# Optimization experiments

Hardware: AMD Instinct MI355X
Metric: run time of the kernel (lower is better)

Reference implementation:

```python
import jax, jax.numpy as jnp
import numpy as np

HIDDEN = 1024
HEADS = 16
HEAD_DIM = HIDDEN // HEADS
B, S = 2, 2048


def setup_inputs() -> dict:
    key = jax.random.key(0)
    k1, k2, k3 = jax.random.split(key, 3)
    scale_in = 1.0 / np.sqrt(HIDDEN)
    x = jax.random.normal(k1, (B, S, HIDDEN), dtype=jnp.float32)
    wqkv_w = jax.random.normal(k2, (3 * HIDDEN, HIDDEN), dtype=jnp.float32) * scale_in
    wo_w = jax.random.normal(k3, (HIDDEN, HIDDEN), dtype=jnp.float32) * scale_in
    wo_b = jnp.zeros((HIDDEN,), dtype=jnp.float32)
    return {"x": x, "wqkv_w": wqkv_w, "wo_w": wo_w, "wo_b": wo_b}


def reference(x, wqkv_w, wo_w, wo_b):
    b, s, d = x.shape
    h, hd = HEADS, HEAD_DIM
    sm_scale = hd ** (-0.5)
    # QKV projection (torch Linear: x @ W^T), then chunk into q,k,v
    qkv = jnp.einsum('bsd,ed->bse', x, wqkv_w)  # [b, s, 3d]
    q, k, v = jnp.split(qkv, 3, axis=-1)
    # [b, h, s, hd]
    q = q.reshape(b, s, h, hd).transpose(0, 2, 1, 3)
    k = k.reshape(b, s, h, hd).transpose(0, 2, 1, 3)
    v = v.reshape(b, s, h, hd).transpose(0, 2, 1, 3)
    # raw scores, then causal mask (mask applied BEFORE scaling, as in source;
    # -inf * scale == -inf so math matches softmax(score*scale) with mask)
    scores = jnp.einsum('bhqe,bhke->bhqk', q, k)
    causal = jnp.tril(jnp.ones((s, s), dtype=bool))
    scores = jnp.where(causal[None, None, :, :], scores, -jnp.inf)
    weights = jax.nn.softmax(scores * sm_scale, axis=-1)
    # dropout p=0.0 (eval) -> identity
    out = jnp.einsum('bhqk,bhke->bhqe', weights, v)
    out = out.transpose(0, 2, 1, 3).reshape(b, s, h * hd)
    y = jnp.einsum('bsd,ed->bse', out, wo_w) + wo_b
    return (y, k, v)
```

## Files before the change

### kernel.cpp

```cpp
#include <hip/hip_runtime.h>
#include <cstdint>
#include <cstddef>


using bf16x8 = __attribute__((ext_vector_type(8))) __bf16;
using f32x4  = __attribute__((ext_vector_type(4))) float;
using u16    = unsigned short;

#define SOFT_SCALE 0.1803368801111244f

__device__ __forceinline__ u16 f2bf(float f) {
  union { float f; uint32_t u; } a; a.f = f;
  uint32_t r = a.u + 0x7fffu + ((a.u >> 16) & 1u);
  return (u16)(r >> 16);
}

__device__ __forceinline__ bf16x8 ldfrag(const u16* p) {
  return *reinterpret_cast<const bf16x8*>(p);
}

__device__ __forceinline__ void gload_lds16(const void* g, void* l) {
  __builtin_amdgcn_global_load_lds((const __attribute__((address_space(1))) void*)g,
                                   (__attribute__((address_space(3))) void*)l,
                                   16, 0, 0);
}

__device__ __forceinline__ uint32_t cvt_pk_bf16(float a, float b) {
  uint32_t r;
  asm("v_cvt_pk_bf16_f32 %0, %1, %2" : "=v"(r) : "v"(a), "v"(b));
  return r;
}

__global__ void cvt_all(const float* __restrict__ x, const float* __restrict__ wqkv,
                        const float* __restrict__ wo,
                        u16* __restrict__ xb, u16* __restrict__ wqkvb, u16* __restrict__ wob) {
  int i = blockIdx.x * blockDim.x + threadIdx.x;
  int stride = gridDim.x * blockDim.x;
  for (; i < 2097152; i += stride) {
    const float* src; u16* dst; int j;
    if (i < 1048576)      { src = x;    dst = xb;    j = i; }
    else if (i < 1835008) { src = wqkv; dst = wqkvb; j = i - 1048576; }
    else                  { src = wo;   dst = wob;   j = i - 1835008; }
    float4 v = reinterpret_cast<const float4*>(src)[j];
    ushort4 o;
    o.x = f2bf(v.x); o.y = f2bf(v.y); o.z = f2bf(v.z); o.w = f2bf(v.w);
    reinterpret_cast<ushort4*>(dst)[j] = o;
  }
}

__global__ __launch_bounds__(512, 2) void qkv_gemm_kernel(
    const u16* __restrict__ Xb, const u16* __restrict__ Wb,
    u16* __restrict__ Qws, u16* __restrict__ Kws, u16* __restrict__ Vtws,
    float* __restrict__ out) {
  extern __shared__ char smem[];

  const int tid = threadIdx.x, lane = tid & 63, wid = tid >> 6;
  const int wr = wid >> 2, wc = wid & 3;
  const int fq = lane >> 4, fr = lane & 15;

  const int wg = (blockIdx.x & 7) * 64 + (blockIdx.x >> 3);
  const int bm = wg >> 4, bn = wg & 15;
  const int m0 = bm * 128, n0 = bn * 192;

  const char* Ab = (const char*)Xb + (size_t)m0 * 2048;
  const char* Bb = (const char*)Wb + (size_t)n0 * 2048;

  f32x4 acc[4][3] = {};

  auto stage_A = [&](int t, int h) {
    char* dst = smem + (t & 1) * 16384 + h * 8192;
    int lin = tid * 16;
    int rl  = lin >> 7;
    int col = (lin & 127) ^ ((rl & 7) << 4);
    gload_lds16(Ab + (size_t)(h * 64 + rl) * 2048 + t * 128 + col, dst + lin);
  };
  auto stage_B = [&](int t) {
    char* dst = smem + 32768 + (t & 1) * 24576;
#pragma unroll
    for (int l = 0; l < 3; ++l) {
      int lin = (l * 512 + tid) * 16;
      int rl  = lin >> 7;
      int col = (lin & 127) ^ ((rl & 7) << 4);
      gload_lds16(Bb + (size_t)rl * 2048 + t * 128 + col, dst + lin);
    }
  };

  stage_A(0, 0); stage_A(0, 1);
  stage_B(0);
  stage_B(1);
  asm volatile("s_waitcnt vmcnt(3)" ::: "memory");
  __builtin_amdgcn_s_barrier();

  bf16x8 afr[2][2];
  bf16x8 bfr[3][2];

  for (int t = 0; t < 16; ++t) {
    const char* As = smem + (t & 1) * 16384;
    const char* Bs = smem + 32768 + (t & 1) * 24576;

#pragma unroll
    for (int m = 0; m < 2; ++m) {
      int row = wr * 64 + m * 16 + fr;
#pragma unroll
      for (int ks = 0; ks < 2; ++ks)
        afr[m][ks] = *(const bf16x8*)(As + row * 128 + ((ks * 64 + fq * 16) ^ ((row & 7) << 4)));
    }
#pragma unroll
    for (int n = 0; n < 3; ++n) {
      int row = wc * 48 + n * 16 + fr;
#pragma unroll
      for (int ks = 0; ks < 2; ++ks)
        bfr[n][ks] = *(const bf16x8*)(Bs + row * 128 + ((ks * 64 + fq * 16) ^ ((row & 7) << 4)));
    }
    if (t + 1 < 16) stage_A(t + 1, 0);
    __builtin_amdgcn_s_barrier();
    asm volatile("s_waitcnt lgkmcnt(0)" ::: "memory");
    __builtin_amdgcn_sched_barrier(0);
    __builtin_amdgcn_s_setprio(1);
#pragma unroll
    for (int m = 0; m < 2; ++m)
#pragma unroll
      for (int n = 0; n < 3; ++n)
#pragma unroll
        for (int ks = 0; ks < 2; ++ks)
          acc[m][n] = __builtin_amdgcn_mfma_f32_16x16x32_bf16(afr[m][ks], bfr[n][ks], acc[m][n], 0, 0, 0);
    __builtin_amdgcn_s_setprio(0);
    __builtin_amdgcn_s_barrier();

#pragma unroll
    for (int m = 0; m < 2; ++m) {
      int row = wr * 64 + (m + 2) * 16 + fr;
#pragma unroll
      for (int ks = 0; ks < 2; ++ks)
        afr[m][ks] = *(const bf16x8*)(As + row * 128 + ((ks * 64 + fq * 16) ^ ((row & 7) << 4)));
    }
    if (t + 1 < 16) stage_A(t + 1, 1);
    if (t + 2 < 16) stage_B(t + 2);
    __builtin_amdgcn_s_barrier();
    asm volatile("s_waitcnt lgkmcnt(0)" ::: "memory");
    __builtin_amdgcn_sched_barrier(0);
    __builtin_amdgcn_s_setprio(1);
#pragma unroll
    for (int m = 0; m < 2; ++m)
#pragma unroll
      for (int n = 0; n < 3; ++n)
#pragma unroll
        for (int ks = 0; ks < 2; ++ks)
          acc[m + 2][n] = __builtin_amdgcn_mfma_f32_16x16x32_bf16(afr[m][ks], bfr[n][ks], acc[m + 2][n], 0, 0, 0);
    __builtin_amdgcn_s_setprio(0);
    if (t < 14)       asm volatile("s_waitcnt vmcnt(3)" ::: "memory");
    else if (t == 14) asm volatile("s_waitcnt vmcnt(0)" ::: "memory");
    __builtin_amdgcn_s_barrier();
  }

  const int mbase = m0 + wr * 64;
#pragma unroll
  for (int m = 0; m < 4; ++m)
#pragma unroll
    for (int n = 0; n < 3; ++n) {
      int mB = mbase + m * 16 + fq * 4;
      int ncol = n0 + wc * 48 + n * 16 + fr;
      int sect = ncol >> 10;
      int nn = ncol & 1023;
      int b = mB >> 11, s0 = mB & 2047;
      int h = nn >> 6, hd = nn & 63;
      size_t base = (((size_t)b * 16 + h) * 2048 + s0) * 64 + hd;
      float v0 = acc[m][n][0], v1 = acc[m][n][1], v2 = acc[m][n][2], v3 = acc[m][n][3];
      if (sect == 0) {
        Qws[base]       = f2bf(v0 * SOFT_SCALE);
        Qws[base + 64]  = f2bf(v1 * SOFT_SCALE);
        Qws[base + 128] = f2bf(v2 * SOFT_SCALE);
        Qws[base + 192] = f2bf(v3 * SOFT_SCALE);
      } else if (sect == 1) {
        Kws[base] = f2bf(v0); Kws[base + 64] = f2bf(v1);
        Kws[base + 128] = f2bf(v2); Kws[base + 192] = f2bf(v3);
        out[4194304 + base] = v0; out[4194304 + base + 64] = v1;
        out[4194304 + base + 128] = v2; out[4194304 + base + 192] = v3;
      } else {
        out[8388608 + base] = v0; out[8388608 + base + 64] = v1;
        out[8388608 + base + 128] = v2; out[8388608 + base + 192] = v3;
        size_t tt = ((size_t)(b * 16 + h) * 64 + hd) * 2048 + s0;
        ushort4 pk; pk.x = f2bf(v0); pk.y = f2bf(v1); pk.z = f2bf(v2); pk.w = f2bf(v3);
        *reinterpret_cast<ushort4*>(Vtws + tt) = pk;
      }
    }
}

__device__ __forceinline__ void gemm128_core(const u16* __restrict__ A,
                                             const u16* __restrict__ B,
                                             int m0, int n0, int K,
                                             u16* As, u16* Bs, f32x4 acc[4][4]) {
  const int tid  = threadIdx.x;
  const int lane = tid & 63;
  const int wid  = tid >> 6;
  const int wr = wid >> 1, wc = wid & 1;
  const int fq = lane >> 4, fr = lane & 15;

  for (int kb = 0; kb < K; kb += 32) {
#pragma unroll
    for (int j = 0; j < 2; ++j) {
      int lin = (j * 256 + tid) * 16;
      int row = lin >> 6;
      int rb  = lin & 63;
      gload_lds16((const char*)(A + (size_t)(m0 + row) * K + kb) + rb, (char*)As + lin);
      gload_lds16((const char*)(B + (size_t)(n0 + row) * K + kb) + rb, (char*)Bs + lin);
    }
    __syncthreads();

    bf16x8 av[4], bv[4];
#pragma unroll
    for (int i = 0; i < 4; ++i) av[i] = ldfrag(As + (wr * 64 + i * 16 + fr) * 32 + fq * 8);
#pragma unroll
    for (int j = 0; j < 4; ++j) bv[j] = ldfrag(Bs + (wc * 64 + j * 16 + fr) * 32 + fq * 8);
    __builtin_amdgcn_s_setprio(1);
#pragma unroll
    for (int i = 0; i < 4; ++i)
#pragma unroll
      for (int j = 0; j < 4; ++j)
        acc[i][j] = __builtin_amdgcn_mfma_f32_16x16x32_bf16(av[i], bv[j], acc[i][j], 0, 0, 0);
    __builtin_amdgcn_s_setprio(0);
    __syncthreads();
  }
}

__global__ __launch_bounds__(256, 4) void attn_kernel(
    const u16* __restrict__ Qw, const u16* __restrict__ Kw,
    const u16* __restrict__ Vtw, u16* __restrict__ Ow) {
  __shared__ u16 Ks[2][64 * 64];
  __shared__ u16 Vs[2][64 * 64];

  const int tid = threadIdx.x, lane = tid & 63, wid = tid >> 6;
  const int wk = wid >> 1, wh = wid & 1;
  const int fq = lane >> 4, fr = lane & 15;
  const int bh = blockIdx.x & 31;
  const int qb = 31 - (blockIdx.x >> 5);
  const int b = bh >> 4, h = bh & 15;
  const int q0 = qb * 64;

  const u16* Qbase  = Qw  + (size_t)bh * 2048 * 64;
  const u16* Kbase  = Kw  + (size_t)bh * 2048 * 64;
  const char* VtBase = (const char*)(Vtw + (size_t)bh * 64 * 2048);

#pragma unroll
  for (int f = 0; f < 2; ++f) {
    int lin = (f * 256 + tid) * 16;
    int row = lin >> 7;
    int logical = lin ^ ((row & 7) << 4);
    gload_lds16((const char*)Kbase + logical, (char*)Ks[0] + lin);
    gload_lds16(VtBase + (size_t)row * 4096 + (logical & 127), (char*)Vs[0] + lin);
  }

  bf16x8 qa[2][2];
#pragma unroll
  for (int qt = 0; qt < 2; ++qt)
#pragma unroll
    for (int kh = 0; kh < 2; ++kh)
      qa[qt][kh] = ldfrag(Qbase + (size_t)(q0 + wh * 32 + qt * 16 + fr) * 64 + kh * 32 + fq * 8);

  float ssum[2] = {0.f, 0.f};
  f32x4 accO[2][4] = {};

  int cur = 0;
  for (int kb = 0; kb <= qb; ++kb) {
    __syncthreads();

    if (kb < qb) {
      const char* kg = (const char*)(Kbase + (size_t)(kb + 1) * 64 * 64);
#pragma unroll
      for (int f = 0; f < 2; ++f) {
        int lin = (f * 256 + tid) * 16;
        int row = lin >> 7;
        int logical = lin ^ ((row & 7) << 4);
        gload_lds16(kg + logical, (char*)Ks[cur ^ 1] + lin);
        gload_lds16(VtBase + (size_t)row * 4096 + (size_t)(kb + 1) * 128 + (logical & 127),
                    (char*)Vs[cur ^ 1] + lin);
      }
    }

    const u16* Kc = Ks[cur];
    const u16* Vc = Vs[cur];

    f32x4 st[2][2];
    __builtin_amdgcn_s_setprio(1);
#pragma unroll
    for (int kvt = 0; kvt < 2; ++kvt) {
      int krow = wk * 32 + kvt * 16 + fr;
      bf16x8 kf0 = ldfrag(Kc + krow * 64 + ((fq * 8)      ^ ((krow & 7) << 3)));
      bf16x8 kf1 = ldfrag(Kc + krow * 64 + ((fq * 8 + 32) ^ ((krow & 7) << 3)));
#pragma unroll
      for (int qt = 0; qt < 2; ++qt) {
        f32x4 z = {};
        z = __builtin_amdgcn_mfma_f32_16x16x32_bf16(kf0, qa[qt][0], z, 0, 0, 0);
        z = __builtin_amdgcn_mfma_f32_16x16x32_bf16(kf1, qa[qt][1], z, 0, 0, 0);
        st[kvt][qt] = z;
      }
    }
    __builtin_amdgcn_s_setprio(0);

    uint32_t W[2][2][2];
#pragma unroll
    for (int qt = 0; qt < 2; ++qt) {
      int qrow = q0 + wh * 32 + qt * 16 + fr;
#pragma unroll
      for (int kvt = 0; kvt < 2; ++kvt) {
        float p0, p1, p2, p3;
        if (kb < qb) {
          p0 = exp2f(st[kvt][qt][0]);
          p1 = exp2f(st[kvt][qt][1]);
          p2 = exp2f(st[kvt][qt][2]);
          p3 = exp2f(st[kvt][qt][3]);
        } else {
          int kvg = kb * 64 + wk * 32 + kvt * 16 + fq * 4;
          p0 = (kvg + 0 > qrow) ? 0.f : exp2f(st[kvt][qt][0]);
          p1 = (kvg + 1 > qrow) ? 0.f : exp2f(st[kvt][qt][1]);
          p2 = (kvg + 2 > qrow) ? 0.f : exp2f(st[kvt][qt][2]);
          p3 = (kvg + 3 > qrow) ? 0.f : exp2f(st[kvt][qt][3]);
        }
        ssum[qt] += (p0 + p1) + (p2 + p3);
        W[qt][kvt][0] = cvt_pk_bf16(p0, p1);
        W[qt][kvt][1] = cvt_pk_bf16(p2, p3);
      }
    }

    union U { uint32_t u[4]; bf16x8 v; };
    U pa[2];
#pragma unroll
    for (int qt = 0; qt < 2; ++qt)
#pragma unroll
      for (int hh = 0; hh < 2; ++hh) {
        uint32_t a0 = W[qt][0][hh], b0 = W[qt][1][hh];
        asm("v_permlane32_swap_b32 %0, %1" : "+v"(a0), "+v"(b0));
        asm("v_permlane16_swap_b32 %0, %1" : "+v"(a0), "+v"(b0));
        pa[qt].u[hh] = a0; pa[qt].u[2 + hh] = b0;
      }

    __builtin_amdgcn_s_setprio(1);
#pragma unroll
    for (int ht = 0; ht < 4; ++ht) {
      int vrow = ht * 16 + fr;
      bf16x8 vb = ldfrag(Vc + vrow * 64 + ((wk * 32 + fq * 8) ^ ((vrow & 7) << 3)));
#pragma unroll
      for (int qt = 0; qt < 2; ++qt)
        accO[qt][ht] = __builtin_amdgcn_mfma_f32_16x16x32_bf16(pa[qt].v, vb, accO[qt][ht], 0, 0, 0);
    }
    __builtin_amdgcn_s_setprio(0);
    cur ^= 1;
  }

#pragma unroll
  for (int qt = 0; qt < 2; ++qt) {
    ssum[qt] += __shfl_xor(ssum[qt], 16);
    ssum[qt] += __shfl_xor(ssum[qt], 32);
  }

  __syncthreads();
  float* Ored = (float*)Ks;
  float* Sred = (float*)Vs;
  if (wk == 1) {
#pragma unroll
    for (int qt = 0; qt < 2; ++qt)
#pragma unroll
      for (int ht = 0; ht < 4; ++ht)
        *reinterpret_cast<f32x4*>(&Ored[(((wh * 2 + qt) * 4 + ht) << 8) + lane * 4]) = accO[qt][ht];
    if (fq == 0) {
      Sred[wh * 64 + fr]      = ssum[0];
      Sred[wh * 64 + 16 + fr] = ssum[1];
    }
  }
  __syncthreads();
  if (wk == 0) {
#pragma unroll
    for (int qt = 0; qt < 2; ++qt)
#pragma unroll
      for (int ht = 0; ht < 4; ++ht) {
        f32x4 o = *reinterpret_cast<const f32x4*>(&Ored[(((wh * 2 + qt) * 4 + ht) << 8) + lane * 4]);
        accO[qt][ht] += o;
      }
    float invq[2][4];
#pragma unroll
    for (int qt = 0; qt < 2; ++qt) {
      float s = ssum[qt] + Sred[wh * 64 + qt * 16 + fr];
      float inv = 1.0f / s;
#pragma unroll
      for (int r = 0; r < 4; ++r) invq[qt][r] = __shfl(inv, fq * 4 + r);
    }
#pragma unroll
    for (int qt = 0; qt < 2; ++qt)
#pragma unroll
      for (int ht = 0; ht < 4; ++ht)
#pragma unroll
        for (int r = 0; r < 4; ++r) {
          float o = accO[qt][ht][r] * invq[qt][r];
          int qr = q0 + wh * 32 + qt * 16 + fq * 4 + r;
          Ow[((size_t)b * 2048 + qr) * 1024 + h * 64 + ht * 16 + fr] = f2bf(o);
        }
  }
}

__global__ __launch_bounds__(256) void proj_gemm_kernel(
    const u16* __restrict__ Ob, const u16* __restrict__ Wob,
    const float* __restrict__ bias, float* __restrict__ out) {
  __shared__ u16 As[128 * 32];
  __shared__ u16 Bs[128 * 32];
  const int NB = 8;
  int m0 = (blockIdx.x / NB) * 128, n0 = (blockIdx.x % NB) * 128;
  f32x4 acc[4][4] = {};
  gemm128_core(Ob, Wob, m0, n0, 1024, As, Bs, acc);

  const int lane = threadIdx.x & 63, wid = threadIdx.x >> 6;
  const int wr = wid >> 1, wc = wid & 1, fq = lane >> 4, fr = lane & 15;
#pragma unroll
  for (int i = 0; i < 4; ++i)
#pragma unroll
    for (int j = 0; j < 4; ++j)
#pragma unroll
      for (int r = 0; r < 4; ++r) {
        int m = m0 + wr * 64 + i * 16 + fq * 4 + r;
        int n = n0 + wc * 64 + j * 16 + fr;
        out[(size_t)m * 1024 + n] = acc[i][j][r] + bias[n];
      }
}

extern "C" void kernel_launch(void* const* d_in, const int* in_sizes, int n_in,
                              void* d_out, int out_size, void* d_ws, size_t ws_size,
                              hipStream_t stream) {
  const float* x    = (const float*)d_in[0];
  const float* wqkv = (const float*)d_in[1];
  const float* wo   = (const float*)d_in[2];
  const float* wo_b = (const float*)d_in[3];
  float* out = (float*)d_out;

  u16* xb    = (u16*)d_ws;
  u16* wqkvb = xb    + 4194304;
  u16* wob   = wqkvb + 3145728;
  u16* q_ws  = wob   + 1048576;
  u16* k_ws  = q_ws  + 4194304;
  u16* vt_ws = k_ws  + 4194304;
  u16* o_ws  = vt_ws + 4194304;

  static bool attr_set = false;
  if (!attr_set) {
    hipFuncSetAttribute((const void*)qkv_gemm_kernel,
                        hipFuncAttributeMaxDynamicSharedMemorySize, 131072);
    attr_set = true;
  }

  cvt_all<<<2048, 256, 0, stream>>>(x, wqkv, wo, xb, wqkvb, wob);
  qkv_gemm_kernel<<<512, 512, 81920, stream>>>(xb, wqkvb, q_ws, k_ws, vt_ws, out);
  attn_kernel<<<32 * 32, 256, 0, stream>>>(q_ws, k_ws, vt_ws, o_ws);
  proj_gemm_kernel<<<32 * 8, 256, 0, stream>>>(o_ws, wob, wo_b, out);
}
```

Measured before the change: 112.6 us.

## Rewrite output projection GEMM with double-buffered swizzled LDS and 8-wave blocks

Replaces the simple single-buffered output projection GEMM with a 512-thread kernel. It uses double-buffered LDS over K tiles of 64, an XOR swizzle to avoid bank conflicts, and a block-index remap for L2 locality. Loads for the next tiles are issued between MFMA phases, with explicit waitcnt and barrier control, so memory latency overlaps compute and the per-iteration sync stalls are gone. This adds complexity and fragile vmcnt bookkeeping, and block count stays at 256.

```diff
diff --git a/kernel.cpp b/kernel.cpp
--- a/kernel.cpp
+++ b/kernel.cpp
@@ -186,43 +186,6 @@
     }
 }
 
-__device__ __forceinline__ void gemm128_core(const u16* __restrict__ A,
-                                             const u16* __restrict__ B,
-                                             int m0, int n0, int K,
-                                             u16* As, u16* Bs, f32x4 acc[4][4]) {
-  const int tid  = threadIdx.x;
-  const int lane = tid & 63;
-  const int wid  = tid >> 6;
-  const int wr = wid >> 1, wc = wid & 1;
-  const int fq = lane >> 4, fr = lane & 15;
-
-  for (int kb = 0; kb < K; kb += 32) {
-#pragma unroll
-    for (int j = 0; j < 2; ++j) {
-      int lin = (j * 256 + tid) * 16;
-      int row = lin >> 6;
-      int rb  = lin & 63;
-      gload_lds16((const char*)(A + (size_t)(m0 + row) * K + kb) + rb, (char*)As + lin);
-      gload_lds16((const char*)(B + (size_t)(n0 + row) * K + kb) + rb, (char*)Bs + lin);
-    }
-    __syncthreads();
-
-    bf16x8 av[4], bv[4];
-#pragma unroll
-    for (int i = 0; i < 4; ++i) av[i] = ldfrag(As + (wr * 64 + i * 16 + fr) * 32 + fq * 8);
-#pragma unroll
-    for (int j = 0; j < 4; ++j) bv[j] = ldfrag(Bs + (wc * 64 + j * 16 + fr) * 32 + fq * 8);
-    __builtin_amdgcn_s_setprio(1);
-#pragma unroll
-    for (int i = 0; i < 4; ++i)
-#pragma unroll
-      for (int j = 0; j < 4; ++j)
-        acc[i][j] = __builtin_amdgcn_mfma_f32_16x16x32_bf16(av[i], bv[j], acc[i][j], 0, 0, 0);
-    __builtin_amdgcn_s_setprio(0);
-    __syncthreads();
-  }
-}
-
 __global__ __launch_bounds__(256, 4) void attn_kernel(
     const u16* __restrict__ Qw, const u16* __restrict__ Kw,
     const u16* __restrict__ Vtw, u16* __restrict__ Ow) {
@@ -397,28 +360,113 @@
   }
 }
 
-__global__ __launch_bounds__(256) void proj_gemm_kernel(
+__global__ __launch_bounds__(512, 2) void proj_gemm_kernel(
     const u16* __restrict__ Ob, const u16* __restrict__ Wob,
     const float* __restrict__ bias, float* __restrict__ out) {
-  __shared__ u16 As[128 * 32];
-  __shared__ u16 Bs[128 * 32];
-  const int NB = 8;
-  int m0 = (blockIdx.x / NB) * 128, n0 = (blockIdx.x % NB) * 128;
-  f32x4 acc[4][4] = {};
-  gemm128_core(Ob, Wob, m0, n0, 1024, As, Bs, acc);
-
-  const int lane = threadIdx.x & 63, wid = threadIdx.x >> 6;
-  const int wr = wid >> 1, wc = wid & 1, fq = lane >> 4, fr = lane & 15;
-#pragma unroll
-  for (int i = 0; i < 4; ++i)
-#pragma unroll
-    for (int j = 0; j < 4; ++j)
-#pragma unroll
-      for (int r = 0; r < 4; ++r) {
-        int m = m0 + wr * 64 + i * 16 + fq * 4 + r;
-        int n = n0 + wc * 64 + j * 16 + fr;
-        out[(size_t)m * 1024 + n] = acc[i][j][r] + bias[n];
-      }
+  extern __shared__ char smem[];
+
+  const int tid = threadIdx.x, lane = tid & 63, wid = tid >> 6;
+  const int wr = wid >> 2, wc = wid & 3;
+  const int fq = lane >> 4, fr = lane & 15;
+
+  const int wg = (blockIdx.x & 7) * 32 + (blockIdx.x >> 3);
+  const int bm = wg >> 3, bn = wg & 7;
+  const int m0 = bm * 128, n0 = bn * 128;
+
+  const char* Ab = (const char*)Ob  + (size_t)m0 * 2048;
+  const char* Bb = (const char*)Wob + (size_t)n0 * 2048;
+
+  f32x4 acc[4][2] = {};
+
+  auto stage = [&](int t, int mat, int h) {
+    char* dst = smem + mat * 32768 + (t & 1) * 16384 + h * 8192;
+    const char* src = mat ? Bb : Ab;
+    int lin = tid * 16;
+    int rl  = lin >> 7;
+    int col = (lin & 127) ^ ((rl & 7) << 4);
+    gload_lds16(src + (size_t)(h * 64 + rl) * 2048 + t * 128 + col, dst + lin);
+  };
+
+  stage(0, 0, 0); stage(0, 0, 1);
+  stage(0, 1, 0); stage(0, 1, 1);
+  stage(1, 1, 0); stage(1, 1, 1);
+  asm volatile("s_waitcnt vmcnt(2)" ::: "memory");
+  __builtin_amdgcn_s_barrier();
+
+  bf16x8 afr[2][2];
+  bf16x8 bfr[2][2];
+
+  for (int t = 0; t < 16; ++t) {
+    const char* As = smem + (t & 1) * 16384;
+    const char* Bs = smem + 32768 + (t & 1) * 16384;
+
+#pragma unroll
+    for (int m = 0; m < 2; ++m) {
+      int row = wr * 64 + m * 16 + fr;
+#pragma unroll
+      for (int ks = 0; ks < 2; ++ks)
+        afr[m][ks] = *(const bf16x8*)(As + row * 128 + ((ks * 64 + fq * 16) ^ ((row & 7) << 4)));
+    }
+#pragma unroll
+    for (int n = 0; n < 2; ++n) {
+      int row = wc * 32 + n * 16 + fr;
+#pragma unroll
+      for (int ks = 0; ks < 2; ++ks)
+        bfr[n][ks] = *(const bf16x8*)(Bs + row * 128 + ((ks * 64 + fq * 16) ^ ((row & 7) << 4)));
+    }
+    if (t + 1 < 16) stage(t + 1, 0, 0);
+    __builtin_amdgcn_s_barrier();
+    asm volatile("s_waitcnt lgkmcnt(0)" ::: "memory");
+    __builtin_amdgcn_sched_barrier(0);
+    __builtin_amdgcn_s_setprio(1);
+#pragma unroll
+    for (int m = 0; m < 2; ++m)
+#pragma unroll
+      for (int n = 0; n < 2; ++n)
+#pragma unroll
+        for (int ks = 0; ks < 2; ++ks)
+          acc[m][n] = __builtin_amdgcn_mfma_f32_16x16x32_bf16(afr[m][ks], bfr[n][ks], acc[m][n], 0, 0, 0);
+    __builtin_amdgcn_s_setprio(0);
+    __builtin_amdgcn_s_barrier();
+
+#pragma unroll
+    for (int m = 0; m < 2; ++m) {
+      int row = wr * 64 + (m + 2) * 16 + fr;
+#pragma unroll
+      for (int ks = 0; ks < 2; ++ks)
+        afr[m][ks] = *(const bf16x8*)(As + row * 128 + ((ks * 64 + fq * 16) ^ ((row & 7) << 4)));
+    }
+    if (t + 1 < 16) stage(t + 1, 0, 1);
+    if (t + 2 < 16) { stage(t + 2, 1, 0); stage(t + 2, 1, 1); }
+    __builtin_amdgcn_s_barrier();
+    asm volatile("s_waitcnt lgkmcnt(0)" ::: "memory");
+    __builtin_amdgcn_sched_barrier(0);
+    __builtin_amdgcn_s_setprio(1);
+#pragma unroll
+    for (int m = 0; m < 2; ++m)
+#pragma unroll
+      for (int n = 0; n < 2; ++n)
+#pragma unroll
+        for (int ks = 0; ks < 2; ++ks)
+          acc[m + 2][n] = __builtin_amdgcn_mfma_f32_16x16x32_bf16(afr[m][ks], bfr[n][ks], acc[m + 2][n], 0, 0, 0);
+    __builtin_amdgcn_s_setprio(0);
+    if (t < 14)       asm volatile("s_waitcnt vmcnt(2)" ::: "memory");
+    else if (t == 14) asm volatile("s_waitcnt vmcnt(0)" ::: "memory");
+    __builtin_amdgcn_s_barrier();
+  }
+
+  const int mbase = m0 + wr * 64;
+#pragma unroll
+  for (int m = 0; m < 4; ++m)
+#pragma unroll
+    for (int n = 0; n < 2; ++n) {
+      int mB = mbase + m * 16 + fq * 4;
+      int ncol = n0 + wc * 32 + n * 16 + fr;
+      float bv = bias[ncol];
+#pragma unroll
+      for (int r = 0; r < 4; ++r)
+        out[(size_t)(mB + r) * 1024 + ncol] = acc[m][n][r] + bv;
+    }
 }
 
 extern "C" void kernel_launch(void* const* d_in, const int* in_sizes, int n_in,
@@ -442,11 +490,13 @@
   if (!attr_set) {
     hipFuncSetAttribute((const void*)qkv_gemm_kernel,
                         hipFuncAttributeMaxDynamicSharedMemorySize, 131072);
+    hipFuncSetAttribute((const void*)proj_gemm_kernel,
+                        hipFuncAttributeMaxDynamicSharedMemorySize, 65536);
     attr_set = true;
   }
 
   cvt_all<<<2048, 256, 0, stream>>>(x, wqkv, wo, xb, wqkvb, wob);
   qkv_gemm_kernel<<<512, 512, 81920, stream>>>(xb, wqkvb, q_ws, k_ws, vt_ws, out);
   attn_kernel<<<32 * 32, 256, 0, stream>>>(q_ws, k_ws, vt_ws, o_ws);
-  proj_gemm_kernel<<<32 * 8, 256, 0, stream>>>(o_ws, wob, wo_b, out);
-}
+  proj_gemm_kernel<<<256, 512, 65536, stream>>>(o_ws, wob, wo_b, out);
+}
```

New measurement: 104.7 us (median of 2 runs). 1.07x faster.
